# Kernel tuning notes

Measured on AMD Instinct MI355X. Metric: run time of the kernel, lower is better.

## Reference

```python
import jax, jax.numpy as jnp
import numpy as np

D_IN = 1024
D_OUT = 1024
NUM_HEADS = 16
HEAD_DIM = D_OUT // NUM_HEADS


def setup_inputs() -> dict:
    key = jax.random.key(0)
    ks = jax.random.split(key, 6)
    scale = 1.0 / np.sqrt(D_IN)
    x = jax.random.normal(ks[0], (4, 2048, D_IN), dtype=jnp.float32)
    # nn.Linear stores weight as [out, in]; we keep [in, out] for x @ W
    W_query = jax.random.uniform(ks[1], (D_IN, D_OUT), jnp.float32, -scale, scale)
    W_key = jax.random.uniform(ks[2], (D_IN, D_OUT), jnp.float32, -scale, scale)
    W_value = jax.random.uniform(ks[3], (D_IN, D_OUT), jnp.float32, -scale, scale)
    W_out = jax.random.uniform(ks[4], (D_OUT, D_OUT), jnp.float32, -scale, scale)
    b_out = jax.random.uniform(ks[5], (D_OUT,), jnp.float32, -scale, scale)
    return {"x": x, "W_query": W_query, "W_key": W_key, "W_value": W_value,
            "W_out": W_out, "b_out": b_out}


def reference(x, W_query, W_key, W_value, W_out, b_out):
    b, n, _ = x.shape
    # QKV projections -> [b, h, n, d]
    def proj(W):
        return (x @ W).reshape(b, n, NUM_HEADS, HEAD_DIM).transpose(0, 2, 1, 3)
    q = proj(W_query)
    k = proj(W_key)
    v = proj(W_value)
    # scaled scores [b, h, n, n] with causal mask
    scores = jnp.einsum('bhqd,bhkd->bhqk', q, k) / jnp.sqrt(jnp.float32(HEAD_DIM))
    causal = jnp.tril(jnp.ones((n, n), dtype=bool))
    scores = jnp.where(causal, scores, -jnp.inf)
    weights = jax.nn.softmax(scores, axis=-1)  # dropout p=0.0 -> identity
    ctx = jnp.einsum('bhqk,bhkd->bhqd', weights, v)
    ctx = ctx.transpose(0, 2, 1, 3).reshape(b, n, D_OUT)
    return ctx @ W_out + b_out
```

## Files before the change

kernel.cpp:

```cpp
#include <hip/hip_runtime.h>
#include <hip/hip_bf16.h>
#include <math.h>


typedef __bf16  bf16x8  __attribute__((ext_vector_type(8)));
typedef __bf16  bf16x2  __attribute__((ext_vector_type(2)));
typedef float   floatx4 __attribute__((ext_vector_type(4)));
typedef short   shortx4 __attribute__((ext_vector_type(4)));

__device__ __forceinline__ unsigned short f2bf(float f) {
    __hip_bfloat16 h = __float2bfloat16(f);
    return *reinterpret_cast<unsigned short*>(&h);
}

__device__ __forceinline__ unsigned int pkbf(float a, float b) {
#if __has_builtin(__builtin_amdgcn_cvt_pk_bf16_f32)
    bf16x2 t = __builtin_amdgcn_cvt_pk_bf16_f32(a, b);
    return __builtin_bit_cast(unsigned int, t);
#else
    return (unsigned int)f2bf(a) | ((unsigned int)f2bf(b) << 16);
#endif
}
__device__ __forceinline__ ushort4 pk4(float a, float b, float c, float d) {
    union { ushort4 u; unsigned int w[2]; } u;
    u.w[0] = pkbf(a, b);
    u.w[1] = pkbf(c, d);
    return u.u;
}

__device__ __forceinline__ void gll16(const unsigned short* g, unsigned short* l) {
    __builtin_amdgcn_global_load_lds(
        (const __attribute__((address_space(1))) unsigned int*)g,
        (__attribute__((address_space(3))) unsigned int*)l, 16, 0, 0);
}

__device__ __forceinline__ int krho(int r) {
    return (r & 0x20) | ((r & 4) << 2) | ((r & 0x18) >> 1) | (r & 3);
}

__global__ void prep(const float* __restrict__ x, unsigned short* __restrict__ xb,
                     const float* __restrict__ Wq, const float* __restrict__ Wk,
                     const float* __restrict__ Wv, const float* __restrict__ Wo,
                     unsigned short* __restrict__ WT, unsigned short* __restrict__ WoT) {
    __shared__ float tile[32][33];
    int bid = blockIdx.x, tid = threadIdx.x;
    if (bid < 8192) {
        int i = (bid * 256 + tid) * 4;
        float4 v = *(const float4*)(x + i);
        *(ushort4*)(xb + i) = pk4(v.x, v.y, v.z, v.w);
        return;
    }
    int id = bid - 8192;
    int mat = id >> 10, rem = id & 1023;
    const float* src = (mat == 0) ? Wq : (mat == 1) ? Wk : (mat == 2) ? Wv : Wo;
    unsigned short* dst = (mat < 3) ? WT : WoT;
    int nbase = (mat < 3) ? mat * 1024 : 0;
    int kt = (rem & 31) * 32, nt = (rem >> 5) * 32;
    int tx = tid & 31, ty = tid >> 5;
    for (int j = 0; j < 32; j += 8)
        tile[ty + j][tx] = src[(kt + ty + j) * 1024 + nt + tx];
    __syncthreads();
    for (int j = 0; j < 32; j += 8) {
        int n = nt + ty + j;
        dst[(nbase + n) * 1024 + kt + tx] = f2bf(tile[tx][ty + j]);
    }
}

template <int EPI, int NBLK>
__global__ __launch_bounds__(256, 3) void gemm_bt(const unsigned short* __restrict__ A,
                                                  const unsigned short* __restrict__ B,
                                                  unsigned short* __restrict__ Qo,
                                                  unsigned short* __restrict__ Ko,
                                                  unsigned short* __restrict__ Vo,
                                                  const float* __restrict__ bias,
                                                  float* __restrict__ Out) {
    __shared__ __align__(16) unsigned short As[2][128 * 64];
    __shared__ __align__(16) unsigned short Bs[2][128 * 64];

    int tid = threadIdx.x;
    int lane = tid & 63, w = tid >> 6;
    int wm = w >> 1, wn = w & 1;
    int lm = lane & 15, quad = lane >> 4;
    int bid = blockIdx.x;
    int xcd = bid & 7, ic = bid >> 3;
    int bm = xcd * 8 + (ic & 7), bn = ic >> 3;
    int m0 = bm * 128, n0 = bn * 128;
    bool sw = (EPI == 1) || (n0 < 2048);

    auto STAGE = [&](int buf, int kb) {
#pragma unroll
        for (int p = 0; p < 4; ++p) {
            int id = p * 256 + tid;
            int row = id >> 3;
            int cbs = ((id & 7) ^ (row & 7)) * 8;
            int lbase = (p * 256 + w * 64) * 8;
            gll16(&A[(m0 + row) * 1024 + kb + cbs], &As[buf][lbase]);
            gll16(&B[(n0 + row) * 1024 + kb + cbs], &Bs[buf][lbase]);
        }
    };

    floatx4 acc[4][4] = {};

    STAGE(0, 0);
    __syncthreads();

#pragma unroll 2
    for (int t = 0; t < 16; ++t) {
        if (t < 15) STAGE((t + 1) & 1, (t + 1) * 64);
        const unsigned short* Ac = &As[t & 1][0];
        const unsigned short* Bc = &Bs[t & 1][0];

        bf16x8 af[2][4], bf[2][4];
        for (int ks = 0; ks < 2; ++ks)
            for (int i = 0; i < 4; ++i) {
                int pu = (((ks * 4 + quad) ^ (lm & 7))) * 8;
                af[ks][i] = *(const bf16x8*)&Ac[(wm * 64 + i * 16 + lm) * 64 + pu];
                bf[ks][i] = *(const bf16x8*)&Bs[t & 1][(wn * 64 + i * 16 + lm) * 64 + pu];
            }
        if (sw) {
            for (int mi = 0; mi < 4; ++mi)
                for (int ni = 0; ni < 4; ++ni) {
                    acc[mi][ni] = __builtin_amdgcn_mfma_f32_16x16x32_bf16(bf[0][ni], af[0][mi], acc[mi][ni], 0, 0, 0);
                    acc[mi][ni] = __builtin_amdgcn_mfma_f32_16x16x32_bf16(bf[1][ni], af[1][mi], acc[mi][ni], 0, 0, 0);
                }
        } else {
            for (int mi = 0; mi < 4; ++mi)
                for (int ni = 0; ni < 4; ++ni) {
                    acc[mi][ni] = __builtin_amdgcn_mfma_f32_16x16x32_bf16(af[0][mi], bf[0][ni], acc[mi][ni], 0, 0, 0);
                    acc[mi][ni] = __builtin_amdgcn_mfma_f32_16x16x32_bf16(af[1][mi], bf[1][ni], acc[mi][ni], 0, 0, 0);
                }
        }
        __syncthreads();
    }

    if constexpr (EPI == 0) {
        if (sw) {
            bool isQ = (n0 < 1024);
            unsigned short* dst = isQ ? Qo : Ko;
            float qs = isQ ? 0.1803368801f : 1.0f;
            for (int mi = 0; mi < 4; ++mi) {
                int s = m0 + wm * 64 + mi * 16 + lm;
                int bb = s >> 11, sl = s & 2047;
                for (int ni = 0; ni < 4; ++ni) {
                    int gcol0 = n0 + wn * 64 + ni * 16 + quad * 4;
                    int h = (gcol0 & 1023) >> 6, d0 = gcol0 & 63;
                    *(ushort4*)&dst[(((size_t)(bb * 16 + h) * 2048) + sl) * 64 + d0] =
                        pk4(acc[mi][ni][0] * qs, acc[mi][ni][1] * qs,
                            acc[mi][ni][2] * qs, acc[mi][ni][3] * qs);
                }
            }
        } else {
            for (int mi = 0; mi < 4; ++mi) {
                int grow0 = m0 + wm * 64 + mi * 16 + quad * 4;
                int bb = grow0 >> 11, sl = grow0 & 2047;
                for (int ni = 0; ni < 4; ++ni) {
                    int gcol = n0 + wn * 64 + ni * 16 + lm;
                    int hn = gcol & 1023;
                    int h = hn >> 6, d = hn & 63;
                    *(ushort4*)&Vo[((size_t)(bb * 16 + h) * 64 + d) * 2048 + sl] =
                        pk4(acc[mi][ni][0], acc[mi][ni][1], acc[mi][ni][2], acc[mi][ni][3]);
                }
            }
        }
    } else {
        for (int mi = 0; mi < 4; ++mi) {
            int s = m0 + wm * 64 + mi * 16 + lm;
            for (int ni = 0; ni < 4; ++ni) {
                int gcol0 = n0 + wn * 64 + ni * 16 + quad * 4;
                float4 bv = *(const float4*)&bias[gcol0];
                float4 o;
                o.x = acc[mi][ni][0] + bv.x; o.y = acc[mi][ni][1] + bv.y;
                o.z = acc[mi][ni][2] + bv.z; o.w = acc[mi][ni][3] + bv.w;
                *(float4*)&Out[(size_t)s * 1024 + gcol0] = o;
            }
        }
    }
}

__global__ __launch_bounds__(512) void attn(const unsigned short* __restrict__ Q,
                                            const unsigned short* __restrict__ K,
                                            const unsigned short* __restrict__ Vt,
                                            unsigned short* __restrict__ ctx) {
    constexpr int LKS = 72;
    __shared__ __align__(16) unsigned short Ks[2][64 * LKS];
    __shared__ __align__(16) unsigned short Vts[2][64 * LKS];

    int tid = threadIdx.x, lane = tid & 63, w = tid >> 6;
    int lm = lane & 15, quad = lane >> 4;
    int blk = blockIdx.x;
    int bh = blk & 63;
    int qt = 15 - (blk >> 6);
    int trips = 2 * qt + 2;
    int tmax = 2 * qt + (w >> 2);
    const unsigned short* Qg  = Q  + (size_t)bh * 2048 * 64;
    const unsigned short* Kg  = K  + (size_t)bh * 2048 * 64;
    const unsigned short* Vtg = Vt + (size_t)bh * 64 * 2048;

    int qrow = qt * 128 + w * 16 + lm;
    bf16x8 aq0 = *(const bf16x8*)&Qg[qrow * 64 + quad * 8];
    bf16x8 aq1 = *(const bf16x8*)&Qg[qrow * 64 + 32 + quad * 8];

    floatx4 O[4] = {};
    float lrow = 0.f;

    int r0 = tid >> 3, c0 = (tid & 7) * 8;
    int rK = krho(r0);

    {
        uint4 k0 = *(const uint4*)&Kg[r0 * 64 + c0];
        uint4 v0 = *(const uint4*)&Vtg[r0 * 2048 + c0];
        *(uint4*)&Ks[0][rK * LKS + c0]  = k0;
        *(uint4*)&Vts[0][r0 * LKS + c0] = v0;
    }
    __syncthreads();

    for (int t = 0; t < trips; ++t) {
        int cur = t & 1, nxt = cur ^ 1;
        bool pre = (t + 1 < trips);
        uint4 pk, pv;
        if (pre) {
            int kb2 = (t + 1) * 64;
            pk = *(const uint4*)&Kg[(kb2 + r0) * 64 + c0];
            pv = *(const uint4*)&Vtg[r0 * 2048 + kb2 + c0];
        }

        if (t <= tmax) {
            const unsigned short* Kc = Ks[cur];
            const unsigned short* Vc = Vts[cur];

            floatx4 s[4];
            __builtin_amdgcn_s_setprio(1);
            for (int n = 0; n < 4; ++n) {
                bf16x8 a0 = *(const bf16x8*)&Kc[(n * 16 + lm) * LKS + quad * 8];
                bf16x8 a1 = *(const bf16x8*)&Kc[(n * 16 + lm) * LKS + 32 + quad * 8];
                floatx4 z = {};
                z = __builtin_amdgcn_mfma_f32_16x16x32_bf16(a0, aq0, z, 0, 0, 0);
                z = __builtin_amdgcn_mfma_f32_16x16x32_bf16(a1, aq1, z, 0, 0, 0);
                s[n] = z;
            }
            __builtin_amdgcn_s_setprio(0);

            bool diag = (t == tmax);
            if (diag) {
                int qr = (w & 3) * 16 + lm;
                for (int n = 0; n < 4; ++n)
                    for (int r = 0; r < 4; ++r) {
                        int kin = (n >> 1) * 32 + (n & 1) * 4 + quad * 8 + r;
                        if (kin > qr) s[n][r] = -INFINITY;
                    }
            }
            float p[4][4], rs = 0.f;
            for (int n = 0; n < 4; ++n)
                for (int r = 0; r < 4; ++r) {
                    p[n][r] = __builtin_amdgcn_exp2f(s[n][r]);
                    rs += p[n][r];
                }
            lrow += rs;

            unsigned int pw[4][2];
            for (int n = 0; n < 4; ++n) {
                pw[n][0] = pkbf(p[n][0], p[n][1]);
                pw[n][1] = pkbf(p[n][2], p[n][3]);
            }
            __builtin_amdgcn_s_setprio(1);
#pragma unroll
            for (int n1 = 0; n1 < 2; ++n1) {
                union { bf16x8 v; unsigned int wd[4]; } pu;
                pu.wd[0] = pw[2 * n1][0];     pu.wd[1] = pw[2 * n1][1];
                pu.wd[2] = pw[2 * n1 + 1][0]; pu.wd[3] = pw[2 * n1 + 1][1];
#pragma unroll
                for (int dblk = 0; dblk < 4; ++dblk) {
                    bf16x8 va = *(const bf16x8*)&Vc[(dblk * 16 + lm) * LKS + n1 * 32 + quad * 8];
                    O[dblk] = __builtin_amdgcn_mfma_f32_16x16x32_bf16(va, pu.v, O[dblk], 0, 0, 0);
                }
            }
            __builtin_amdgcn_s_setprio(0);
        }

        if (pre) {
            *(uint4*)&Ks[nxt][rK * LKS + c0]  = pk;
            *(uint4*)&Vts[nxt][r0 * LKS + c0] = pv;
        }
        __syncthreads();
    }

    lrow += __shfl_xor(lrow, 16);
    lrow += __shfl_xor(lrow, 32);

    int b = bh >> 4, h = bh & 15;
    int q = qt * 128 + w * 16 + lm;
    float inv = 1.0f / lrow;
    for (int dblk = 0; dblk < 4; ++dblk) {
        *(ushort4*)&ctx[((size_t)(b * 2048 + q)) * 1024 + h * 64 + dblk * 16 + quad * 4] =
            pk4(O[dblk][0] * inv, O[dblk][1] * inv, O[dblk][2] * inv, O[dblk][3] * inv);
    }
}

extern "C" void kernel_launch(void* const* d_in, const int* in_sizes, int n_in,
                              void* d_out, int out_size, void* d_ws, size_t ws_size,
                              hipStream_t stream) {
    const float* x   = (const float*)d_in[0];
    const float* Wq  = (const float*)d_in[1];
    const float* Wk  = (const float*)d_in[2];
    const float* Wv  = (const float*)d_in[3];
    const float* Wo  = (const float*)d_in[4];
    const float* bo  = (const float*)d_in[5];
    float* out = (float*)d_out;

    char* ws = (char*)d_ws;
    unsigned short* xb  = (unsigned short*)(ws);
    unsigned short* WT  = (unsigned short*)(ws + 16777216);
    unsigned short* WoT = (unsigned short*)(ws + 23068672);
    unsigned short* Qb  = (unsigned short*)(ws + 25165824);
    unsigned short* Kb  = (unsigned short*)(ws + 41943040);
    unsigned short* Vtb = (unsigned short*)(ws + 58720256);
    unsigned short* ctx = xb;

    prep<<<12288, 256, 0, stream>>>(x, xb, Wq, Wk, Wv, Wo, WT, WoT);
    gemm_bt<0, 24><<<1536, 256, 0, stream>>>(xb, WT, Qb, Kb, Vtb, nullptr, nullptr);
    attn<<<1024, 512, 0, stream>>>(Qb, Kb, Vtb, ctx);
    gemm_bt<1, 8><<<512, 256, 0, stream>>>(ctx, WoT, nullptr, nullptr, nullptr, bo, out);
}
```

Measured before the change: 231.5 us.

## Switch GEMM to triple-buffered BK=32 pipeline with fine-grained vmcnt waits

Reworks the projection GEMM main loop from a double-buffered K-tile of 64 to a triple-buffered K-tile of 32, prefetching two stages ahead. The generic __syncthreads is replaced by explicit s_waitcnt vmcnt(4)/lgkmcnt(0) plus s_barrier, so the latest prefetch can stay in flight across the barrier. LDS use drops, which may help occupancy, but the loop runs twice as many iterations with half the MFMA work each and twice as many barriers.

```diff
diff --git a/kernel.cpp b/kernel.cpp
--- a/kernel.cpp
+++ b/kernel.cpp
@@ -74,8 +74,8 @@
                                                   unsigned short* __restrict__ Vo,
                                                   const float* __restrict__ bias,
                                                   float* __restrict__ Out) {
-    __shared__ __align__(16) unsigned short As[2][128 * 64];
-    __shared__ __align__(16) unsigned short Bs[2][128 * 64];
+    __shared__ __align__(16) unsigned short As[3][128 * 32];
+    __shared__ __align__(16) unsigned short Bs[3][128 * 32];
 
     int tid = threadIdx.x;
     int lane = tid & 63, w = tid >> 6;
@@ -89,10 +89,10 @@
 
     auto STAGE = [&](int buf, int kb) {
 #pragma unroll
-        for (int p = 0; p < 4; ++p) {
+        for (int p = 0; p < 2; ++p) {
             int id = p * 256 + tid;
-            int row = id >> 3;
-            int cbs = ((id & 7) ^ (row & 7)) * 8;
+            int row = id >> 2;
+            int cbs = ((id & 3) ^ (row & 3)) * 8;
             int lbase = (p * 256 + w * 64) * 8;
             gll16(&A[(m0 + row) * 1024 + kb + cbs], &As[buf][lbase]);
             gll16(&B[(n0 + row) * 1024 + kb + cbs], &Bs[buf][lbase]);
@@ -102,35 +102,48 @@
     floatx4 acc[4][4] = {};
 
     STAGE(0, 0);
-    __syncthreads();
-
-#pragma unroll 2
-    for (int t = 0; t < 16; ++t) {
-        if (t < 15) STAGE((t + 1) & 1, (t + 1) * 64);
-        const unsigned short* Ac = &As[t & 1][0];
-        const unsigned short* Bc = &Bs[t & 1][0];
-
-        bf16x8 af[2][4], bf[2][4];
-        for (int ks = 0; ks < 2; ++ks)
-            for (int i = 0; i < 4; ++i) {
-                int pu = (((ks * 4 + quad) ^ (lm & 7))) * 8;
-                af[ks][i] = *(const bf16x8*)&Ac[(wm * 64 + i * 16 + lm) * 64 + pu];
-                bf[ks][i] = *(const bf16x8*)&Bs[t & 1][(wn * 64 + i * 16 + lm) * 64 + pu];
-            }
+    STAGE(1, 32);
+    asm volatile("s_waitcnt vmcnt(4)" ::: "memory");
+    __builtin_amdgcn_s_barrier();
+    asm volatile("" ::: "memory");
+
+    int cur = 0, stg = 2;
+#pragma unroll 1
+    for (int t = 0; t < 32; ++t) {
+        if (t + 2 < 32) STAGE(stg, (t + 2) * 32);
+
+        const unsigned short* Ac = &As[cur][0];
+        const unsigned short* Bc = &Bs[cur][0];
+        bf16x8 af[4], bf[4];
+#pragma unroll
+        for (int i = 0; i < 4; ++i) {
+            int pu = (quad ^ (lm & 3)) * 8;
+            af[i] = *(const bf16x8*)&Ac[(wm * 64 + i * 16 + lm) * 32 + pu];
+            bf[i] = *(const bf16x8*)&Bc[(wn * 64 + i * 16 + lm) * 32 + pu];
+        }
         if (sw) {
+#pragma unroll
             for (int mi = 0; mi < 4; ++mi)
-                for (int ni = 0; ni < 4; ++ni) {
-                    acc[mi][ni] = __builtin_amdgcn_mfma_f32_16x16x32_bf16(bf[0][ni], af[0][mi], acc[mi][ni], 0, 0, 0);
-                    acc[mi][ni] = __builtin_amdgcn_mfma_f32_16x16x32_bf16(bf[1][ni], af[1][mi], acc[mi][ni], 0, 0, 0);
-                }
+#pragma unroll
+                for (int ni = 0; ni < 4; ++ni)
+                    acc[mi][ni] = __builtin_amdgcn_mfma_f32_16x16x32_bf16(bf[ni], af[mi], acc[mi][ni], 0, 0, 0);
         } else {
+#pragma unroll
             for (int mi = 0; mi < 4; ++mi)
-                for (int ni = 0; ni < 4; ++ni) {
-                    acc[mi][ni] = __builtin_amdgcn_mfma_f32_16x16x32_bf16(af[0][mi], bf[0][ni], acc[mi][ni], 0, 0, 0);
-                    acc[mi][ni] = __builtin_amdgcn_mfma_f32_16x16x32_bf16(af[1][mi], bf[1][ni], acc[mi][ni], 0, 0, 0);
-                }
-        }
-        __syncthreads();
+#pragma unroll
+                for (int ni = 0; ni < 4; ++ni)
+                    acc[mi][ni] = __builtin_amdgcn_mfma_f32_16x16x32_bf16(af[mi], bf[ni], acc[mi][ni], 0, 0, 0);
+        }
+
+        if (t < 31) {
+            asm volatile("s_waitcnt lgkmcnt(0)" ::: "memory");
+            if (t < 30) { asm volatile("s_waitcnt vmcnt(4)" ::: "memory"); }
+            else        { asm volatile("s_waitcnt vmcnt(0)" ::: "memory"); }
+            __builtin_amdgcn_s_barrier();
+            asm volatile("" ::: "memory");
+        }
+        if (++cur == 3) cur = 0;
+        if (++stg == 3) stg = 0;
     }
 
     if constexpr (EPI == 0) {
```

Measured after the change: 274.2 us. 1.18x slower.
